# Kernel optimization log

Hardware: AMD Instinct MI355X
Metric: run time of the kernel (lower is better)

The kernel has to match this reference:

```python
import jax, jax.numpy as jnp
import numpy as np

N = 50000      # nodes
E = 800000     # edges (avg degree 16)
D = 128        # hidden_channels
FFN = 512
BOT = 64
L = 3          # number of stacked GCN layers


def setup_inputs() -> dict:
    key = jax.random.key(0)
    ks = jax.random.split(key, 10)
    x = jax.random.normal(ks[0], (N, D), dtype=jnp.float32)
    edge_index = jax.random.randint(ks[1], (2, E), 0, N, dtype=jnp.int64)
    s = np.float32(1.0 / np.sqrt(D))
    conv_W = jax.random.normal(ks[2], (L, D, D), dtype=jnp.float32) * s
    conv_b = jnp.zeros((L, D), dtype=jnp.float32)
    fc1_w = jax.random.normal(ks[3], (D, FFN), dtype=jnp.float32) * s
    fc1_b = jnp.zeros((FFN,), dtype=jnp.float32)
    fc2_w = jax.random.normal(ks[4], (FFN, BOT), dtype=jnp.float32) * np.float32(1.0 / np.sqrt(FFN))
    fc2_b = jnp.zeros((BOT,), dtype=jnp.float32)
    return {"x": x, "edge_index": edge_index, "conv_W": conv_W, "conv_b": conv_b,
            "fc1_w": fc1_w, "fc1_b": fc1_b, "fc2_w": fc2_w, "fc2_b": fc2_b}


def _gcn_conv(x, src, dst, W, b):
    """GCNConv: D^{-1/2} (A+I) D^{-1/2} X W + b, degree computed with self-loops."""
    n = x.shape[0]
    deg = jax.ops.segment_sum(jnp.ones(src.shape[0], x.dtype), dst, num_segments=n) + 1.0
    norm = jax.lax.rsqrt(deg)                      # [N]
    xw = x @ W                                     # [N, D] transform before scatter
    coef = (norm[src] * norm[dst])[:, None]        # [E, 1]
    agg = jax.ops.segment_sum(xw[src] * coef, dst, num_segments=n)  # gather-scale-scatter
    return agg + xw * (norm * norm)[:, None] + b   # self-loop term + bias


def reference(x, edge_index, conv_W, conv_b, fc1_w, fc1_b, fc2_w, fc2_b):
    src, dst = edge_index[0], edge_index[1]
    for l in range(L):
        x = jax.nn.relu(_gcn_conv(x, src, dst, conv_W[l], conv_b[l]))
        # dropout = identity in eval mode
    x = jax.nn.relu(x @ fc1_w + fc1_b)
    return x @ fc2_w + fc2_b
```

## Files before the change

kernel.cpp:

```cpp
#include <hip/hip_runtime.h>
#include <hip/hip_fp16.h>

#define D 128
#define FFN 512
#define BOT 64
#define EPB 4096

typedef _Float16 f16x8 __attribute__((ext_vector_type(8)));
typedef float f32x4 __attribute__((ext_vector_type(4)));


__global__ __launch_bounds__(256) void k_bcnt(const int* __restrict__ dst, int* __restrict__ bcnt, int nE) {
  __shared__ int h[256];
  int t = threadIdx.x;
  h[t] = 0;
  __syncthreads();
  int base = blockIdx.x * EPB;
  #pragma unroll
  for (int m = 0; m < EPB / 256; ++m) {
    int idx = base + m * 256 + t;
    if (idx < nE) atomicAdd(&h[dst[idx] >> 8], 1);
  }
  __syncthreads();
  if (h[t] > 0) atomicAdd(&bcnt[t], h[t]);
}

__global__ __launch_bounds__(256) void k_bscan(const int* __restrict__ bcnt, int* __restrict__ boff,
                                               int* __restrict__ bcur, int nbkt, int nE) {
  __shared__ int s[256];
  int t = threadIdx.x;
  int v = (t < nbkt) ? bcnt[t] : 0;
  s[t] = v;
  __syncthreads();
  for (int d = 1; d < 256; d <<= 1) {
    int add = (t >= d) ? s[t - d] : 0;
    __syncthreads();
    s[t] += add;
    __syncthreads();
  }
  int ex = s[t] - v;
  boff[t] = ex;
  bcur[t] = ex;
  if (t == 255) boff[256] = nE;
  if (t >= nbkt) boff[t] = nE;
}

__global__ __launch_bounds__(256) void k_bscatter(const int* __restrict__ ei, int* __restrict__ bcur,
                                                  uint2* __restrict__ bed, int nE) {
  __shared__ uint2 st[EPB];
  __shared__ int cnt[256], off[256], base[256], cur[256];
  int t = threadIdx.x;
  int blk0 = blockIdx.x * EPB;
  int nblk = nE - blk0;
  if (nblk > EPB) nblk = EPB;

  cnt[t] = 0;
  cur[t] = 0;
  __syncthreads();

  int rs[EPB / 256], rd[EPB / 256];
  #pragma unroll
  for (int m = 0; m < EPB / 256; ++m) {
    int idx = blk0 + m * 256 + t;
    if (idx < nE) {
      rs[m] = ei[idx];
      rd[m] = ei[nE + idx];
      atomicAdd(&cnt[rd[m] >> 8], 1);
    } else {
      rd[m] = -1;
    }
  }
  __syncthreads();

  int v = cnt[t];
  off[t] = v;
  __syncthreads();
  for (int d = 1; d < 256; d <<= 1) {
    int add = (t >= d) ? off[t - d] : 0;
    __syncthreads();
    off[t] += add;
    __syncthreads();
  }
  int ex = off[t] - v;
  __syncthreads();
  off[t] = ex;
  base[t] = (v > 0) ? atomicAdd(&bcur[t], v) : 0;
  __syncthreads();

  #pragma unroll
  for (int m = 0; m < EPB / 256; ++m) {
    if (rd[m] >= 0) {
      int b = rd[m] >> 8;
      int p = off[b] + atomicAdd(&cur[b], 1);
      st[p] = make_uint2((unsigned)rs[m], (unsigned)rd[m]);
    }
  }
  __syncthreads();

  for (int j = t; j < nblk; j += 256) {
    uint2 pr = st[j];
    int b = (int)(pr.y >> 8);
    bed[base[b] + (j - off[b])] = pr;
  }
}

__global__ __launch_bounds__(256) void k_bcsr(const uint2* __restrict__ bed, const int* __restrict__ boff,
                                              int* __restrict__ rowptr, float* __restrict__ nrm,
                                              int* __restrict__ col, int N, int nE) {
  __shared__ int cnt[256], noff[256], cur[256];
  int t = threadIdx.x;
  int b = blockIdx.x;
  int e0 = boff[b], e1 = boff[b + 1];

  cnt[t] = 0;
  __syncthreads();
  for (int j = e0 + t; j < e1; j += 256)
    atomicAdd(&cnt[bed[j].y & 255], 1);
  __syncthreads();

  int v = cnt[t];
  noff[t] = v;
  __syncthreads();
  for (int d = 1; d < 256; d <<= 1) {
    int add = (t >= d) ? noff[t - d] : 0;
    __syncthreads();
    noff[t] += add;
    __syncthreads();
  }
  int ex = noff[t] - v;
  __syncthreads();
  noff[t] = ex;
  cur[t] = ex;
  __syncthreads();

  int node = (b << 8) + t;
  if (node < N) {
    rowptr[node] = e0 + ex;
    nrm[node] = rsqrtf((float)v + 1.0f);
  }
  if (b == 0 && t == 0) rowptr[N] = nE;

  for (int j = e0 + t; j < e1; j += 256) {
    uint2 pr = bed[j];
    int d2 = (int)(pr.y & 255);
    int p = atomicAdd(&cur[d2], 1);
    col[e0 + p] = (int)pr.x;
  }
}


__global__ __launch_bounds__(256) void k_split(const float* __restrict__ X,
                                               __half* __restrict__ Xh, __half* __restrict__ Xl, int n8) {
  int i = blockIdx.x * 256 + threadIdx.x;
  if (i >= n8) return;
  float4 a = ((const float4*)X)[i * 2];
  float4 b = ((const float4*)X)[i * 2 + 1];
  float v[8] = {a.x, a.y, a.z, a.w, b.x, b.y, b.z, b.w};
  __half2 hh[4], ll[4];
  #pragma unroll
  for (int q = 0; q < 4; ++q) {
    __half h0 = __float2half_rn(v[2 * q]);
    __half h1 = __float2half_rn(v[2 * q + 1]);
    __half l0 = __float2half_rn(v[2 * q] - __half2float(h0));
    __half l1 = __float2half_rn(v[2 * q + 1] - __half2float(h1));
    hh[q] = __halves2half2(h0, h1);
    ll[q] = __halves2half2(l0, l1);
  }
  *(uint4*)(Xh + (size_t)i * 8) = *(uint4*)hh;
  *(uint4*)(Xl + (size_t)i * 8) = *(uint4*)ll;
}

__global__ __launch_bounds__(256) void k_splitw(const float* __restrict__ W,
                                                __half* __restrict__ WhT, __half* __restrict__ WlT,
                                                int K, int N) {
  int id = blockIdx.x * 256 + threadIdx.x;
  if (id >= K * N) return;
  int n = id / K, k = id % K;
  float v = W[(size_t)k * N + n];
  __half h = __float2half_rn(v);
  WhT[id] = h;
  WlT[id] = __float2half_rn(v - __half2float(h));
}

__global__ __launch_bounds__(256) void k_splitwc(const float* __restrict__ W,
                                                 __half* __restrict__ WhT, __half* __restrict__ WlT,
                                                 int total) {
  int id = blockIdx.x * 256 + threadIdx.x;
  if (id >= total) return;
  int l = id / (D * D), r = id % (D * D);
  int n = r / D, k = r % D;
  float v = W[(size_t)l * D * D + (size_t)k * D + n];
  __half h = __float2half_rn(v);
  WhT[id] = h;
  WlT[id] = __float2half_rn(v - __half2float(h));
}


__global__ __launch_bounds__(256, 4)
void k_conv(const __half* __restrict__ Ah_g, const __half* __restrict__ Al_g,
            const __half* __restrict__ BhT_g, const __half* __restrict__ BlT_g,
            const float* __restrict__ aux, __half* __restrict__ Yo, int M) {
  __shared__ __half Ahs[64][40];
  __shared__ __half Als[64][40];
  __shared__ __half Bhs[128][40];
  __shared__ __half Bls[128][40];

  const int t = threadIdx.x;
  const int rbase = blockIdx.x * 64;
  const int lane = t & 63, wid = t >> 6;
  const int wr = (wid >> 1) * 32;
  const int wc = (wid & 1) * 64;
  const int lr = lane & 15, lq = lane >> 4;

  f32x4 acc[2][4];
  #pragma unroll
  for (int m = 0; m < 2; ++m)
    #pragma unroll
    for (int n = 0; n < 4; ++n) acc[m][n] = (f32x4){0.f, 0.f, 0.f, 0.f};

  for (int kc = 0; kc < D; kc += 32) {
    __syncthreads();
    {
      int row = t >> 2, q = t & 3;
      int gr = rbase + row;
      uint4 vh = {0, 0, 0, 0}, vl = {0, 0, 0, 0};
      if (gr < M) {
        vh = *(const uint4*)(Ah_g + (size_t)gr * D + kc + q * 8);
        vl = *(const uint4*)(Al_g + (size_t)gr * D + kc + q * 8);
      }
      *(uint4*)&Ahs[row][q * 8] = vh;
      *(uint4*)&Als[row][q * 8] = vl;
    }
    #pragma unroll
    for (int mm = 0; mm < 2; ++mm) {
      int idx = mm * 256 + t;
      int c = idx >> 2, q = idx & 3;
      size_t src = (size_t)c * D + kc + q * 8;
      *(uint4*)&Bhs[c][q * 8] = *(const uint4*)(BhT_g + src);
      *(uint4*)&Bls[c][q * 8] = *(const uint4*)(BlT_g + src);
    }
    __syncthreads();

    f16x8 fa[2], fal[2], fb[4], fbl[4];
    #pragma unroll
    for (int m = 0; m < 2; ++m) {
      fa[m]  = *(const f16x8*)&Ahs[wr + m * 16 + lr][lq * 8];
      fal[m] = *(const f16x8*)&Als[wr + m * 16 + lr][lq * 8];
    }
    #pragma unroll
    for (int n = 0; n < 4; ++n) {
      fb[n]  = *(const f16x8*)&Bhs[wc + n * 16 + lr][lq * 8];
      fbl[n] = *(const f16x8*)&Bls[wc + n * 16 + lr][lq * 8];
    }
    #pragma unroll
    for (int m = 0; m < 2; ++m)
      #pragma unroll
      for (int n = 0; n < 4; ++n) {
        acc[m][n] = __builtin_amdgcn_mfma_f32_16x16x32_f16(fa[m], fb[n], acc[m][n], 0, 0, 0);
        acc[m][n] = __builtin_amdgcn_mfma_f32_16x16x32_f16(fa[m], fbl[n], acc[m][n], 0, 0, 0);
        acc[m][n] = __builtin_amdgcn_mfma_f32_16x16x32_f16(fal[m], fb[n], acc[m][n], 0, 0, 0);
      }
  }

  #pragma unroll
  for (int m = 0; m < 2; ++m)
    #pragma unroll
    for (int j = 0; j < 4; ++j) {
      int row = rbase + wr + m * 16 + lq * 4 + j;
      if (row < M) {
        float s = aux[row];
        #pragma unroll
        for (int n = 0; n < 4; ++n) {
          int colg = wc + n * 16 + lr;
          Yo[(size_t)row * D + colg] = __float2half_rn(acc[m][n][j] * s);
        }
      }
    }
}


__global__ __launch_bounds__(256, 3)
void k_mlp(const __half* __restrict__ Xh_g, const __half* __restrict__ Xl_g,
           const __half* __restrict__ W1hT, const __half* __restrict__ W1lT,
           const float* __restrict__ B1,
           const __half* __restrict__ W2hT, const __half* __restrict__ W2lT,
           const float* __restrict__ B2,
           float* __restrict__ Out, int M) {
  __shared__ __half Xhs[64][40], Xls[64][40];
  __shared__ __half W1hs[64][40], W1ls[64][40];
  __shared__ __half Hs[2][64][40];
  __shared__ __half W2hs[2][64][40], W2ls[2][64][40];

  const int t = threadIdx.x;
  const int rbase = blockIdx.x * 64;
  const int lane = t & 63, wid = t >> 6;
  const int wr = (wid >> 1) * 32;
  const int wcn = (wid & 1) * 32;
  const int lr = lane & 15, lq = lane >> 4;

  f32x4 accO[2][2];
  #pragma unroll
  for (int m = 0; m < 2; ++m)
    #pragma unroll
    for (int n = 0; n < 2; ++n) accO[m][n] = (f32x4){0.f, 0.f, 0.f, 0.f};

  for (int ch = 0; ch < FFN / 64; ++ch) {
    f32x4 accH[2][2];
    #pragma unroll
    for (int m = 0; m < 2; ++m)
      #pragma unroll
      for (int n = 0; n < 2; ++n) accH[m][n] = (f32x4){0.f, 0.f, 0.f, 0.f};

    for (int kc = 0; kc < D; kc += 32) {
      __syncthreads();
      {
        int row = t >> 2, q = t & 3;
        int gr = rbase + row;
        uint4 vh = {0, 0, 0, 0}, vl = {0, 0, 0, 0};
        if (gr < M) {
          vh = *(const uint4*)(Xh_g + (size_t)gr * D + kc + q * 8);
          vl = *(const uint4*)(Xl_g + (size_t)gr * D + kc + q * 8);
        }
        *(uint4*)&Xhs[row][q * 8] = vh;
        *(uint4*)&Xls[row][q * 8] = vl;
      }
      {
        int c = t >> 2, q = t & 3;
        size_t src = (size_t)(ch * 64 + c) * D + kc + q * 8;
        *(uint4*)&W1hs[c][q * 8] = *(const uint4*)(W1hT + src);
        *(uint4*)&W1ls[c][q * 8] = *(const uint4*)(W1lT + src);
      }
      __syncthreads();

      f16x8 fa[2], fal[2], fb[2], fbl[2];
      #pragma unroll
      for (int m = 0; m < 2; ++m) {
        fa[m]  = *(const f16x8*)&Xhs[wr + m * 16 + lr][lq * 8];
        fal[m] = *(const f16x8*)&Xls[wr + m * 16 + lr][lq * 8];
      }
      #pragma unroll
      for (int n = 0; n < 2; ++n) {
        fb[n]  = *(const f16x8*)&W1hs[wcn + n * 16 + lr][lq * 8];
        fbl[n] = *(const f16x8*)&W1ls[wcn + n * 16 + lr][lq * 8];
      }
      #pragma unroll
      for (int m = 0; m < 2; ++m)
        #pragma unroll
        for (int n = 0; n < 2; ++n) {
          accH[m][n] = __builtin_amdgcn_mfma_f32_16x16x32_f16(fa[m], fb[n], accH[m][n], 0, 0, 0);
          accH[m][n] = __builtin_amdgcn_mfma_f32_16x16x32_f16(fa[m], fbl[n], accH[m][n], 0, 0, 0);
          accH[m][n] = __builtin_amdgcn_mfma_f32_16x16x32_f16(fal[m], fb[n], accH[m][n], 0, 0, 0);
        }
    }

    __syncthreads();
    {
      float bb1[2];
      #pragma unroll
      for (int n = 0; n < 2; ++n) bb1[n] = B1[ch * 64 + wcn + n * 16 + lr];
      #pragma unroll
      for (int m = 0; m < 2; ++m)
        #pragma unroll
        for (int n = 0; n < 2; ++n)
          #pragma unroll
          for (int j = 0; j < 4; ++j) {
            int rl = wr + m * 16 + lq * 4 + j;
            int cl = wcn + n * 16 + lr;
            Hs[cl >> 5][rl][cl & 31] = __float2half_rn(fmaxf(accH[m][n][j] + bb1[n], 0.f));
          }
    }
    #pragma unroll
    for (int s = 0; s < 2; ++s) {
      int c = t >> 2, q = t & 3;
      size_t src = (size_t)c * FFN + ch * 64 + s * 32 + q * 8;
      *(uint4*)&W2hs[s][c][q * 8] = *(const uint4*)(W2hT + src);
      *(uint4*)&W2ls[s][c][q * 8] = *(const uint4*)(W2lT + src);
    }
    __syncthreads();

    #pragma unroll
    for (int s = 0; s < 2; ++s) {
      f16x8 fha[2], fwb[2], fwbl[2];
      #pragma unroll
      for (int m = 0; m < 2; ++m)
        fha[m] = *(const f16x8*)&Hs[s][wr + m * 16 + lr][lq * 8];
      #pragma unroll
      for (int n = 0; n < 2; ++n) {
        fwb[n]  = *(const f16x8*)&W2hs[s][wcn + n * 16 + lr][lq * 8];
        fwbl[n] = *(const f16x8*)&W2ls[s][wcn + n * 16 + lr][lq * 8];
      }
      #pragma unroll
      for (int m = 0; m < 2; ++m)
        #pragma unroll
        for (int n = 0; n < 2; ++n) {
          accO[m][n] = __builtin_amdgcn_mfma_f32_16x16x32_f16(fha[m], fwb[n], accO[m][n], 0, 0, 0);
          accO[m][n] = __builtin_amdgcn_mfma_f32_16x16x32_f16(fha[m], fwbl[n], accO[m][n], 0, 0, 0);
        }
    }
  }

  #pragma unroll
  for (int m = 0; m < 2; ++m)
    #pragma unroll
    for (int j = 0; j < 4; ++j) {
      int row = rbase + wr + m * 16 + lq * 4 + j;
      if (row < M) {
        #pragma unroll
        for (int n = 0; n < 2; ++n) {
          int colg = wcn + n * 16 + lr;
          Out[(size_t)row * BOT + colg] = accO[m][n][j] + B2[colg];
        }
      }
    }
}


__global__ __launch_bounds__(256) void k_agg(const __half* __restrict__ Y,
                                             const int* __restrict__ rowptr, const int* __restrict__ col,
                                             const float* __restrict__ nrm, const float* __restrict__ bias,
                                             __half* __restrict__ Xh, __half* __restrict__ Xl, int n) {
  int gtid = blockIdx.x * 256 + threadIdx.x;
  int node = gtid >> 5;
  int sl = threadIdx.x & 31;
  if (node >= n) return;
  const uint2* Yv = (const uint2*)Y;

  auto up = [](uint2 v, float4& a) {
    __half2 h0 = *(__half2*)&v.x, h1 = *(__half2*)&v.y;
    float2 f0 = __half22float2(h0), f1 = __half22float2(h1);
    a.x += f0.x; a.y += f0.y; a.z += f1.x; a.w += f1.y;
  };

  float4 s0 = {0.f, 0.f, 0.f, 0.f}, s1 = {0.f, 0.f, 0.f, 0.f};
  float4 s2 = {0.f, 0.f, 0.f, 0.f}, s3 = {0.f, 0.f, 0.f, 0.f};
  up(Yv[(size_t)node * 32 + sl], s0);
  int e0 = rowptr[node], e1 = rowptr[node + 1];
  int e = e0;
  for (; e + 4 <= e1; e += 4) {
    int c0 = col[e], c1 = col[e + 1], c2 = col[e + 2], c3 = col[e + 3];
    uint2 v0 = Yv[(size_t)c0 * 32 + sl];
    uint2 v1 = Yv[(size_t)c1 * 32 + sl];
    uint2 v2 = Yv[(size_t)c2 * 32 + sl];
    uint2 v3 = Yv[(size_t)c3 * 32 + sl];
    up(v0, s0); up(v1, s1); up(v2, s2); up(v3, s3);
  }
  for (; e < e1; ++e) up(Yv[(size_t)col[e] * 32 + sl], s0);

  float4 s;
  s.x = (s0.x + s1.x) + (s2.x + s3.x);
  s.y = (s0.y + s1.y) + (s2.y + s3.y);
  s.z = (s0.z + s1.z) + (s2.z + s3.z);
  s.w = (s0.w + s1.w) + (s2.w + s3.w);

  float nm = nrm[node];
  float4 bb = ((const float4*)bias)[sl];
  float o[4];
  o[0] = fmaxf(fmaf(s.x, nm, bb.x), 0.f);
  o[1] = fmaxf(fmaf(s.y, nm, bb.y), 0.f);
  o[2] = fmaxf(fmaf(s.z, nm, bb.z), 0.f);
  o[3] = fmaxf(fmaf(s.w, nm, bb.w), 0.f);

  __half h[4], l[4];
  #pragma unroll
  for (int q = 0; q < 4; ++q) {
    h[q] = __float2half_rn(o[q]);
    l[q] = __float2half_rn(o[q] - __half2float(h[q]));
  }
  uint2 ph, pl;
  ph.x = *(unsigned*)&(*(__half2*)&h[0]);
  __half2 h23 = __halves2half2(h[2], h[3]);
  ph.y = *(unsigned*)&h23;
  __half2 l01 = __halves2half2(l[0], l[1]);
  __half2 l23 = __halves2half2(l[2], l[3]);
  pl.x = *(unsigned*)&l01;
  pl.y = *(unsigned*)&l23;
  __half2 h01 = __halves2half2(h[0], h[1]);
  ph.x = *(unsigned*)&h01;
  ((uint2*)Xh)[(size_t)node * 32 + sl] = ph;
  ((uint2*)Xl)[(size_t)node * 32 + sl] = pl;
}

extern "C" void kernel_launch(void* const* d_in, const int* in_sizes, int n_in,
                              void* d_out, int out_size, void* d_ws, size_t ws_size,
                              hipStream_t stream) {
  const float* x     = (const float*)d_in[0];
  const int*   ei    = (const int*)d_in[1];
  const float* convW = (const float*)d_in[2];
  const float* convB = (const float*)d_in[3];
  const float* w1    = (const float*)d_in[4];
  const float* b1    = (const float*)d_in[5];
  const float* w2    = (const float*)d_in[6];
  const float* b2    = (const float*)d_in[7];
  float* out = (float*)d_out;

  int N = in_sizes[0] / D;
  int E = in_sizes[1] / 2;
  int L = in_sizes[2] / (D * D);
  int NBKT = (N + 255) >> 8;

  char* ws = (char*)d_ws;
  size_t off = 0;
  auto alloc = [&](size_t bytes) -> char* {
    char* p = ws + off;
    off += (bytes + 255) & ~(size_t)255;
    return p;
  };
  float*  nrm    = (float*)alloc((size_t)N * 4);
  int*    rowptr = (int*)alloc((size_t)(N + 1) * 4);
  int*    col    = (int*)alloc((size_t)E * 4);
  int*    bcnt   = (int*)alloc(512 * 4);
  int*    boff   = (int*)alloc(512 * 4);
  int*    bcur   = (int*)alloc(512 * 4);
  uint2*  bed    = (uint2*)alloc((size_t)E * 8);
  __half* Xh     = (__half*)alloc((size_t)N * D * 2);
  __half* Xl     = (__half*)alloc((size_t)N * D * 2);
  __half* Yh     = (__half*)alloc((size_t)N * D * 2);
  __half* WcTh   = (__half*)alloc((size_t)L * D * D * 2);
  __half* WcTl   = (__half*)alloc((size_t)L * D * D * 2);
  __half* W1Th   = (__half*)alloc((size_t)D * FFN * 2);
  __half* W1Tl   = (__half*)alloc((size_t)D * FFN * 2);
  __half* W2Th   = (__half*)alloc((size_t)FFN * BOT * 2);
  __half* W2Tl   = (__half*)alloc((size_t)FFN * BOT * 2);

  int gS = (E + EPB - 1) / EPB;
  hipMemsetAsync(bcnt, 0, 512 * 4, stream);
  k_bcnt<<<gS, 256, 0, stream>>>(ei + E, bcnt, E);
  k_bscan<<<1, 256, 0, stream>>>(bcnt, boff, bcur, NBKT, E);
  k_bscatter<<<gS, 256, 0, stream>>>(ei, bcur, bed, E);
  k_bcsr<<<NBKT, 256, 0, stream>>>(bed, boff, rowptr, nrm, col, N, E);

  int n8 = N * D / 8;
  k_split<<<(n8 + 255) / 256, 256, 0, stream>>>(x, Xh, Xl, n8);
  k_splitwc<<<(L * D * D + 255) / 256, 256, 0, stream>>>(convW, WcTh, WcTl, L * D * D);
  k_splitw<<<(D * FFN + 255) / 256, 256, 0, stream>>>(w1, W1Th, W1Tl, D, FFN);
  k_splitw<<<(FFN * BOT + 255) / 256, 256, 0, stream>>>(w2, W2Th, W2Tl, FFN, BOT);

  int nRB = (N + 63) / 64;
  for (int l = 0; l < L; ++l) {
    k_conv<<<nRB, 256, 0, stream>>>(
        Xh, Xl, WcTh + (size_t)l * D * D, WcTl + (size_t)l * D * D, nrm, Yh, N);
    k_agg<<<(N * 32 + 255) / 256, 256, 0, stream>>>(Yh, rowptr, col, nrm, convB + (size_t)l * D,
                                                    Xh, Xl, N);
  }

  k_mlp<<<nRB, 256, 0, stream>>>(Xh, Xl, W1Th, W1Tl, b1, W2Th, W2Tl, b2, out, N);
}
```

Measured before the change: 271.0 us.

## Stage full-K tiles in MLP kernel and widen aggregation loads to 16 bytes

The MLP kernel now loads each block's whole 64x128 X tile into shared memory once, instead of reloading it for every FFN chunk. It also loads the full W1 chunk per iteration, which removes the inner k-loop and its barriers, and reuses one weight buffer for both W1 and W2. Occupancy is lowered from 3 to 2 blocks to make room for the larger shared-memory footprint. The aggregation kernel switches to 16 lanes per node with 16-byte gathers and two accumulator sets, halving the thread count and widening each memory transaction, at the cost of more registers per thread.

```diff
diff --git a/kernel.cpp b/kernel.cpp
--- a/kernel.cpp
+++ b/kernel.cpp
@@ -279,17 +279,16 @@
 }
 
 
-__global__ __launch_bounds__(256, 3)
+__global__ __launch_bounds__(256, 2)
 void k_mlp(const __half* __restrict__ Xh_g, const __half* __restrict__ Xl_g,
            const __half* __restrict__ W1hT, const __half* __restrict__ W1lT,
            const float* __restrict__ B1,
            const __half* __restrict__ W2hT, const __half* __restrict__ W2lT,
            const float* __restrict__ B2,
            float* __restrict__ Out, int M) {
-  __shared__ __half Xhs[64][40], Xls[64][40];
-  __shared__ __half W1hs[64][40], W1ls[64][40];
-  __shared__ __half Hs[2][64][40];
-  __shared__ __half W2hs[2][64][40], W2ls[2][64][40];
+  __shared__ __half Xhs[64][136], Xls[64][136];
+  __shared__ __half Ws[2][64][136];
+  __shared__ __half Hs[64][72];
 
   const int t = threadIdx.x;
   const int rbase = blockIdx.x * 64;
@@ -298,6 +297,20 @@
   const int wcn = (wid & 1) * 32;
   const int lr = lane & 15, lq = lane >> 4;
 
+  #pragma unroll
+  for (int mm = 0; mm < 4; ++mm) {
+    int idx = mm * 256 + t;
+    int row = idx >> 4, q = idx & 15;
+    int gr = rbase + row;
+    uint4 vh = {0, 0, 0, 0}, vl = {0, 0, 0, 0};
+    if (gr < M) {
+      vh = *(const uint4*)(Xh_g + (size_t)gr * D + q * 8);
+      vl = *(const uint4*)(Xl_g + (size_t)gr * D + q * 8);
+    }
+    *(uint4*)&Xhs[row][q * 8] = vh;
+    *(uint4*)&Xls[row][q * 8] = vl;
+  }
+
   f32x4 accO[2][2];
   #pragma unroll
   for (int m = 0; m < 2; ++m)
@@ -305,43 +318,35 @@
     for (int n = 0; n < 2; ++n) accO[m][n] = (f32x4){0.f, 0.f, 0.f, 0.f};
 
   for (int ch = 0; ch < FFN / 64; ++ch) {
+    __syncthreads();
+    #pragma unroll
+    for (int mm = 0; mm < 4; ++mm) {
+      int idx = mm * 256 + t;
+      int c = idx >> 4, q = idx & 15;
+      size_t src = (size_t)(ch * 64 + c) * D + q * 8;
+      *(uint4*)&Ws[0][c][q * 8] = *(const uint4*)(W1hT + src);
+      *(uint4*)&Ws[1][c][q * 8] = *(const uint4*)(W1lT + src);
+    }
+    __syncthreads();
+
     f32x4 accH[2][2];
     #pragma unroll
     for (int m = 0; m < 2; ++m)
       #pragma unroll
       for (int n = 0; n < 2; ++n) accH[m][n] = (f32x4){0.f, 0.f, 0.f, 0.f};
 
-    for (int kc = 0; kc < D; kc += 32) {
-      __syncthreads();
-      {
-        int row = t >> 2, q = t & 3;
-        int gr = rbase + row;
-        uint4 vh = {0, 0, 0, 0}, vl = {0, 0, 0, 0};
-        if (gr < M) {
-          vh = *(const uint4*)(Xh_g + (size_t)gr * D + kc + q * 8);
-          vl = *(const uint4*)(Xl_g + (size_t)gr * D + kc + q * 8);
-        }
-        *(uint4*)&Xhs[row][q * 8] = vh;
-        *(uint4*)&Xls[row][q * 8] = vl;
-      }
-      {
-        int c = t >> 2, q = t & 3;
-        size_t src = (size_t)(ch * 64 + c) * D + kc + q * 8;
-        *(uint4*)&W1hs[c][q * 8] = *(const uint4*)(W1hT + src);
-        *(uint4*)&W1ls[c][q * 8] = *(const uint4*)(W1lT + src);
-      }
-      __syncthreads();
-
+    #pragma unroll
+    for (int kf = 0; kf < 4; ++kf) {
       f16x8 fa[2], fal[2], fb[2], fbl[2];
       #pragma unroll
       for (int m = 0; m < 2; ++m) {
-        fa[m]  = *(const f16x8*)&Xhs[wr + m * 16 + lr][lq * 8];
-        fal[m] = *(const f16x8*)&Xls[wr + m * 16 + lr][lq * 8];
+        fa[m]  = *(const f16x8*)&Xhs[wr + m * 16 + lr][kf * 32 + lq * 8];
+        fal[m] = *(const f16x8*)&Xls[wr + m * 16 + lr][kf * 32 + lq * 8];
       }
       #pragma unroll
       for (int n = 0; n < 2; ++n) {
-        fb[n]  = *(const f16x8*)&W1hs[wcn + n * 16 + lr][lq * 8];
-        fbl[n] = *(const f16x8*)&W1ls[wcn + n * 16 + lr][lq * 8];
+        fb[n]  = *(const f16x8*)&Ws[0][wcn + n * 16 + lr][kf * 32 + lq * 8];
+        fbl[n] = *(const f16x8*)&Ws[1][wcn + n * 16 + lr][kf * 32 + lq * 8];
       }
       #pragma unroll
       for (int m = 0; m < 2; ++m)
@@ -353,7 +358,6 @@
         }
     }
 
-    __syncthreads();
     {
       float bb1[2];
       #pragma unroll
@@ -366,15 +370,17 @@
           for (int j = 0; j < 4; ++j) {
             int rl = wr + m * 16 + lq * 4 + j;
             int cl = wcn + n * 16 + lr;
-            Hs[cl >> 5][rl][cl & 31] = __float2half_rn(fmaxf(accH[m][n][j] + bb1[n], 0.f));
+            Hs[rl][cl] = __float2half_rn(fmaxf(accH[m][n][j] + bb1[n], 0.f));
           }
     }
-    #pragma unroll
-    for (int s = 0; s < 2; ++s) {
-      int c = t >> 2, q = t & 3;
-      size_t src = (size_t)c * FFN + ch * 64 + s * 32 + q * 8;
-      *(uint4*)&W2hs[s][c][q * 8] = *(const uint4*)(W2hT + src);
-      *(uint4*)&W2ls[s][c][q * 8] = *(const uint4*)(W2lT + src);
+    __syncthreads();
+    #pragma unroll
+    for (int mm = 0; mm < 2; ++mm) {
+      int idx = mm * 256 + t;
+      int c = idx >> 3, q = idx & 7;
+      size_t src = (size_t)c * FFN + ch * 64 + q * 8;
+      *(uint4*)&Ws[0][c][q * 8] = *(const uint4*)(W2hT + src);
+      *(uint4*)&Ws[1][c][q * 8] = *(const uint4*)(W2lT + src);
     }
     __syncthreads();
 
@@ -383,11 +389,11 @@
       f16x8 fha[2], fwb[2], fwbl[2];
       #pragma unroll
       for (int m = 0; m < 2; ++m)
-        fha[m] = *(const f16x8*)&Hs[s][wr + m * 16 + lr][lq * 8];
+        fha[m] = *(const f16x8*)&Hs[wr + m * 16 + lr][s * 32 + lq * 8];
       #pragma unroll
       for (int n = 0; n < 2; ++n) {
-        fwb[n]  = *(const f16x8*)&W2hs[s][wcn + n * 16 + lr][lq * 8];
-        fwbl[n] = *(const f16x8*)&W2ls[s][wcn + n * 16 + lr][lq * 8];
+        fwb[n]  = *(const f16x8*)&Ws[0][wcn + n * 16 + lr][s * 32 + lq * 8];
+        fwbl[n] = *(const f16x8*)&Ws[1][wcn + n * 16 + lr][s * 32 + lq * 8];
       }
       #pragma unroll
       for (int m = 0; m < 2; ++m)
@@ -420,64 +426,46 @@
                                              const float* __restrict__ nrm, const float* __restrict__ bias,
                                              __half* __restrict__ Xh, __half* __restrict__ Xl, int n) {
   int gtid = blockIdx.x * 256 + threadIdx.x;
-  int node = gtid >> 5;
-  int sl = threadIdx.x & 31;
+  int node = gtid >> 4;
+  int sl = threadIdx.x & 15;
   if (node >= n) return;
-  const uint2* Yv = (const uint2*)Y;
-
-  auto up = [](uint2 v, float4& a) {
-    __half2 h0 = *(__half2*)&v.x, h1 = *(__half2*)&v.y;
-    float2 f0 = __half22float2(h0), f1 = __half22float2(h1);
-    a.x += f0.x; a.y += f0.y; a.z += f1.x; a.w += f1.y;
+  const uint4* Yv = (const uint4*)Y;
+
+  float s0[8] = {0.f, 0.f, 0.f, 0.f, 0.f, 0.f, 0.f, 0.f};
+  float s1[8] = {0.f, 0.f, 0.f, 0.f, 0.f, 0.f, 0.f, 0.f};
+  auto up = [](uint4 v, float* a) {
+    __half2* hp = (__half2*)&v;
+    #pragma unroll
+    for (int q = 0; q < 4; ++q) {
+      float2 f = __half22float2(hp[q]);
+      a[2 * q] += f.x;
+      a[2 * q + 1] += f.y;
+    }
   };
-
-  float4 s0 = {0.f, 0.f, 0.f, 0.f}, s1 = {0.f, 0.f, 0.f, 0.f};
-  float4 s2 = {0.f, 0.f, 0.f, 0.f}, s3 = {0.f, 0.f, 0.f, 0.f};
-  up(Yv[(size_t)node * 32 + sl], s0);
+  up(Yv[(size_t)node * 16 + sl], s0);
   int e0 = rowptr[node], e1 = rowptr[node + 1];
   int e = e0;
   for (; e + 4 <= e1; e += 4) {
     int c0 = col[e], c1 = col[e + 1], c2 = col[e + 2], c3 = col[e + 3];
-    uint2 v0 = Yv[(size_t)c0 * 32 + sl];
-    uint2 v1 = Yv[(size_t)c1 * 32 + sl];
-    uint2 v2 = Yv[(size_t)c2 * 32 + sl];
-    uint2 v3 = Yv[(size_t)c3 * 32 + sl];
-    up(v0, s0); up(v1, s1); up(v2, s2); up(v3, s3);
-  }
-  for (; e < e1; ++e) up(Yv[(size_t)col[e] * 32 + sl], s0);
-
-  float4 s;
-  s.x = (s0.x + s1.x) + (s2.x + s3.x);
-  s.y = (s0.y + s1.y) + (s2.y + s3.y);
-  s.z = (s0.z + s1.z) + (s2.z + s3.z);
-  s.w = (s0.w + s1.w) + (s2.w + s3.w);
+    uint4 v0 = Yv[(size_t)c0 * 16 + sl];
+    uint4 v1 = Yv[(size_t)c1 * 16 + sl];
+    uint4 v2 = Yv[(size_t)c2 * 16 + sl];
+    uint4 v3 = Yv[(size_t)c3 * 16 + sl];
+    up(v0, s0); up(v1, s1); up(v2, s0); up(v3, s1);
+  }
+  for (; e < e1; ++e) up(Yv[(size_t)col[e] * 16 + sl], s0);
 
   float nm = nrm[node];
-  float4 bb = ((const float4*)bias)[sl];
-  float o[4];
-  o[0] = fmaxf(fmaf(s.x, nm, bb.x), 0.f);
-  o[1] = fmaxf(fmaf(s.y, nm, bb.y), 0.f);
-  o[2] = fmaxf(fmaf(s.z, nm, bb.z), 0.f);
-  o[3] = fmaxf(fmaf(s.w, nm, bb.w), 0.f);
-
-  __half h[4], l[4];
-  #pragma unroll
-  for (int q = 0; q < 4; ++q) {
-    h[q] = __float2half_rn(o[q]);
-    l[q] = __float2half_rn(o[q] - __half2float(h[q]));
-  }
-  uint2 ph, pl;
-  ph.x = *(unsigned*)&(*(__half2*)&h[0]);
-  __half2 h23 = __halves2half2(h[2], h[3]);
-  ph.y = *(unsigned*)&h23;
-  __half2 l01 = __halves2half2(l[0], l[1]);
-  __half2 l23 = __halves2half2(l[2], l[3]);
-  pl.x = *(unsigned*)&l01;
-  pl.y = *(unsigned*)&l23;
-  __half2 h01 = __halves2half2(h[0], h[1]);
-  ph.x = *(unsigned*)&h01;
-  ((uint2*)Xh)[(size_t)node * 32 + sl] = ph;
-  ((uint2*)Xl)[(size_t)node * 32 + sl] = pl;
+  const float* bp = bias + sl * 8;
+  __half h[8], l[8];
+  #pragma unroll
+  for (int q = 0; q < 8; ++q) {
+    float o = fmaxf(fmaf(s0[q] + s1[q], nm, bp[q]), 0.f);
+    h[q] = __float2half_rn(o);
+    l[q] = __float2half_rn(o - __half2float(h[q]));
+  }
+  ((uint4*)Xh)[(size_t)node * 16 + sl] = *(uint4*)h;
+  ((uint4*)Xl)[(size_t)node * 16 + sl] = *(uint4*)l;
 }
 
 extern "C" void kernel_launch(void* const* d_in, const int* in_sizes, int n_in,
@@ -539,7 +527,7 @@
   for (int l = 0; l < L; ++l) {
     k_conv<<<nRB, 256, 0, stream>>>(
         Xh, Xl, WcTh + (size_t)l * D * D, WcTl + (size_t)l * D * D, nrm, Yh, N);
-    k_agg<<<(N * 32 + 255) / 256, 256, 0, stream>>>(Yh, rowptr, col, nrm, convB + (size_t)l * D,
+    k_agg<<<(N * 16 + 255) / 256, 256, 0, stream>>>(Yh, rowptr, col, nrm, convB + (size_t)l * D,
                                                     Xh, Xl, N);
   }
 
```

Result: faster. 252.4 us (-6.9%).
